# Performance work log

Measured on AMD Instinct MI355X. Metric: run time of the kernel, lower is better.

## Reference

```python
import jax, jax.numpy as jnp
import numpy as np

N_HEADS = 12


def setup_inputs() -> dict:
    key = jax.random.key(0)
    ks = jax.random.split(key, 4)
    B, S, D = 2, 2048, 768
    x = jax.random.normal(ks[0], (B, S, D), dtype=jnp.float32)
    # nn.Linear-style init scale ~ 1/sqrt(D) to keep logits reasonable
    scale = 1.0 / np.sqrt(D)
    Wq = jax.random.normal(ks[1], (D, D), dtype=jnp.float32) * scale
    Wk = jax.random.normal(ks[2], (D, D), dtype=jnp.float32) * scale
    Wv = jax.random.normal(ks[3], (D, D), dtype=jnp.float32) * scale
    bq = jnp.zeros((D,), jnp.float32)
    bk = jnp.zeros((D,), jnp.float32)
    bv = jnp.zeros((D,), jnp.float32)
    mask = jnp.ones((B, S), jnp.int32)
    return {"x": x, "Wq": Wq, "bq": bq, "Wk": Wk, "bk": bk,
            "Wv": Wv, "bv": bv, "mask": mask}


def reference(x, Wq, bq, Wk, bk, Wv, bv, mask):
    B, S, D = x.shape
    H = N_HEADS
    W = D // H
    # q,k,v: (B,S,D) -> (B,H,S,W)
    def proj(Wm, bm):
        return (x @ Wm.T + bm).reshape(B, S, H, W).transpose(0, 2, 1, 3)
    q, k, v = proj(Wq, bq), proj(Wk, bk), proj(Wv, bv)
    scores = jnp.einsum("bhsw,bhtw->bhst", q, k) / jnp.sqrt(
        jnp.asarray(W, x.dtype))
    # mask: (B,S) -> broadcast over query positions; 0 -> -1e20
    scores = jnp.where(mask[:, None, None, :] == 0,
                       jnp.asarray(-1e20, scores.dtype), scores)
    attn = jax.nn.softmax(scores, axis=-1)  # (B,H,S,S)
    # dropout p=0.0 (eval) -> identity
    ctx = jnp.einsum("bhst,bhtw->bhsw", attn, v)
    hidden = ctx.transpose(0, 2, 1, 3).reshape(B, S, D)
    return hidden
```

## Files before the change

### kernel.cpp

```cpp
#include <hip/hip_runtime.h>
#include <hip/hip_bf16.h>
#include <stdint.h>


typedef __attribute__((ext_vector_type(8))) short bf16x8;
typedef __attribute__((ext_vector_type(4))) float f32x4;
typedef __attribute__((ext_vector_type(16))) float f32x16;
typedef __attribute__((ext_vector_type(8))) unsigned short u16x8;

#define MFMA16(a, b, c) __builtin_amdgcn_mfma_f32_16x16x32_bf16((a), (b), (c), 0, 0, 0)
#define MFMA32(a, b, c) __builtin_amdgcn_mfma_f32_32x32x16_bf16((a), (b), (c), 0, 0, 0)
#define SWZ(row, colb) ((colb) ^ (((row) & 7) << 4))

union U32x4BF {
  unsigned u[4];
  bf16x8 v;
};

__device__ __forceinline__ void gl_lds16(const void* g, void* l) {
  __builtin_amdgcn_global_load_lds(
      (__attribute__((address_space(1))) void*)const_cast<void*>(g),
      (__attribute__((address_space(3))) void*)l, 16, 0, 0);
}

__device__ __forceinline__ unsigned short f2bf(float x) {
  unsigned int v = __float_as_uint(x);
  return (unsigned short)((v + 0x7fffu + ((v >> 16) & 1u)) >> 16);
}

__global__ __launch_bounds__(256) void cvt_all(
    const float* __restrict__ x, const float* __restrict__ wq,
    const float* __restrict__ wk, const float* __restrict__ wv,
    unsigned short* __restrict__ xb, unsigned short* __restrict__ wb) {
  int i = blockIdx.x * 256 + threadIdx.x;
  const float* s;
  unsigned short* d;
  int off;
  if (i < 393216)      { s = x;  d = xb;            off = i; }
  else if (i < 466944) { s = wq; d = wb;            off = i - 393216; }
  else if (i < 540672) { s = wk; d = wb + 589824;   off = i - 466944; }
  else                 { s = wv; d = wb + 1179648;  off = i - 540672; }
  const float4* sp = (const float4*)s + (size_t)off * 2;
  float4 a = sp[0], b2 = sp[1];
  u16x8 o;
  o[0] = f2bf(a.x); o[1] = f2bf(a.y); o[2] = f2bf(a.z); o[3] = f2bf(a.w);
  o[4] = f2bf(b2.x); o[5] = f2bf(b2.y); o[6] = f2bf(b2.z); o[7] = f2bf(b2.w);
  *((u16x8*)d + off) = o;
}

__global__ __launch_bounds__(256) void proj_gemm(
    const unsigned short* __restrict__ xb, const unsigned short* __restrict__ wb,
    const float* __restrict__ bq, const float* __restrict__ bk, const float* __restrict__ bv,
    unsigned short* __restrict__ qw, unsigned short* __restrict__ kw,
    unsigned short* __restrict__ vw) {
  __shared__ unsigned short lA[128 * 64];
  __shared__ unsigned short lB[128 * 64];
  const int t = threadIdx.x, lane = t & 63, wave = t >> 6;
  const int wr = wave >> 1, wc = wave & 1;
  const int mbase = blockIdx.x * 128;
  const int wsel = blockIdx.y / 6;
  const int nbase = (blockIdx.y % 6) * 128;
  const unsigned short* wmat = wb + (size_t)wsel * 589824;

  f32x4 acc[4][4];
#pragma unroll
  for (int i = 0; i < 4; i++)
#pragma unroll
    for (int j = 0; j < 4; j++) acc[i][j] = (f32x4){0.f, 0.f, 0.f, 0.f};

  char* lAc = (char*)lA;
  char* lBc = (char*)lB;

  for (int kt = 0; kt < 768; kt += 64) {
#pragma unroll
    for (int i = 0; i < 4; i++) {
      int p = t * 16 + i * 4096;
      int row = p >> 7, colb = p & 127;
      int scol = SWZ(row, colb);
      gl_lds16((const char*)xb + ((size_t)(mbase + row) * 768 + kt) * 2 + scol, lAc + p);
      gl_lds16((const char*)wmat + ((size_t)(nbase + row) * 768 + kt) * 2 + scol, lBc + p);
    }
    __syncthreads();

    bf16x8 af[2][4], bff[2][4];
#pragma unroll
    for (int mf = 0; mf < 4; mf++) {
      int row = wr * 64 + mf * 16 + (lane & 15);
#pragma unroll
      for (int kk = 0; kk < 2; kk++)
        af[kk][mf] = *(const bf16x8*)(lAc + row * 128 + SWZ(row, kk * 64 + (lane >> 4) * 16));
    }
#pragma unroll
    for (int nf = 0; nf < 4; nf++) {
      int row = wc * 64 + nf * 16 + (lane & 15);
#pragma unroll
      for (int kk = 0; kk < 2; kk++)
        bff[kk][nf] = *(const bf16x8*)(lBc + row * 128 + SWZ(row, kk * 64 + (lane >> 4) * 16));
    }
    if (wsel == 2) {
#pragma unroll
      for (int kk = 0; kk < 2; kk++)
#pragma unroll
        for (int mf = 0; mf < 4; mf++)
#pragma unroll
          for (int nf = 0; nf < 4; nf++)
            acc[mf][nf] = MFMA16(bff[kk][nf], af[kk][mf], acc[mf][nf]);
    } else {
#pragma unroll
      for (int kk = 0; kk < 2; kk++)
#pragma unroll
        for (int mf = 0; mf < 4; mf++)
#pragma unroll
          for (int nf = 0; nf < 4; nf++)
            acc[mf][nf] = MFMA16(af[kk][mf], bff[kk][nf], acc[mf][nf]);
    }
    __syncthreads();
  }

  const float QSCALE = 0.125f * 1.44269504089f;
  if (wsel == 2) {
#pragma unroll
    for (int nf = 0; nf < 4; nf++) {
#pragma unroll
      for (int mf = 0; mf < 4; mf++) {
#pragma unroll
        for (int r = 0; r < 4; r++) {
          int n = nbase + wc * 64 + nf * 16 + (lane >> 4) * 4 + r;
          int m = mbase + wr * 64 + mf * 16 + (lane & 15);
          int b_ = m >> 11, s = m & 2047;
          int h = n >> 6, wcol = n & 63;
          float val = acc[mf][nf][r] + bv[n];
          vw[(((size_t)b_ * 12 + h) * 64 + wcol) * 2048 + s] = f2bf(val);
        }
      }
    }
  } else {
    const float* bias = (wsel == 0) ? bq : bk;
#pragma unroll
    for (int nf = 0; nf < 4; nf++) {
      int n = nbase + wc * 64 + nf * 16 + (lane & 15);
      float bv_ = bias[n];
      int h = n >> 6, wcol = n & 63;
#pragma unroll
      for (int mf = 0; mf < 4; mf++) {
#pragma unroll
        for (int r = 0; r < 4; r++) {
          int m = mbase + wr * 64 + mf * 16 + (lane >> 4) * 4 + r;
          int b_ = m >> 11, s = m & 2047;
          float val = acc[mf][nf][r] + bv_;
          size_t bhh = (size_t)b_ * 12 + h;
          if (wsel == 0)
            qw[(bhh * 2048 + s) * 64 + wcol] = f2bf(val * QSCALE);
          else
            kw[(bhh * 2048 + s) * 64 + wcol] = f2bf(val);
        }
      }
    }
  }
}

__global__ __launch_bounds__(256, 4) void attn_kernel(
    const unsigned short* __restrict__ qw, const unsigned short* __restrict__ kw,
    const unsigned short* __restrict__ vw, const int* __restrict__ mask,
    float* __restrict__ out) {
  __shared__ __align__(16) char smem[33536];
  const int t = threadIdx.x, lane = t & 63, wave = t >> 6;
  const int wq = wave >> 1, wk = wave & 1;
  const int l31 = lane & 31, hl = lane >> 5;
  const int qb = blockIdx.x, bh = blockIdx.y;
  const int b = bh / 12, hh = bh - b * 12;

  {
    const int* mb = mask + (size_t)b * 2048 + t * 8;
    int4 a0 = *(const int4*)mb;
    int4 a1 = *(const int4*)(mb + 4);
    unsigned by = (unsigned)(a0.x != 0) | ((unsigned)(a0.y != 0) << 1) |
                  ((unsigned)(a0.z != 0) << 2) | ((unsigned)(a0.w != 0) << 3) |
                  ((unsigned)(a1.x != 0) << 4) | ((unsigned)(a1.y != 0) << 5) |
                  ((unsigned)(a1.z != 0) << 6) | ((unsigned)(a1.w != 0) << 7);
    smem[32768 + t] = (char)by;
  }

  bf16x8 qv[4];
  {
    int qrow = qb * 64 + wq * 32 + l31;
    const char* qp = (const char*)qw + ((size_t)bh * 2048 + qrow) * 128 + hl * 16;
#pragma unroll
    for (int s = 0; s < 4; s++) qv[s] = *(const bf16x8*)(qp + s * 32);
  }

  const char* kbaseg = (const char*)kw + (size_t)bh * 262144;
  const char* vbaseg = (const char*)vw + (size_t)bh * 262144;

  const int p0 = t * 16, p1 = t * 16 + 4096;
  const int r0 = p0 >> 7, s0 = SWZ(r0, p0 & 127);
  const int r1 = p1 >> 7, s1 = SWZ(r1, p1 & 127);

#define STAGE(IT, BUF)                                                                   \
  do {                                                                                   \
    int it_ = (IT);                                                                      \
    gl_lds16(kbaseg + (size_t)it_ * 8192 + r0 * 128 + s0, smem + (BUF) * 8192 + p0);     \
    gl_lds16(vbaseg + (size_t)r0 * 4096 + it_ * 128 + s0, smem + 16384 + (BUF) * 8192 + p0); \
    gl_lds16(kbaseg + (size_t)it_ * 8192 + r1 * 128 + s1, smem + (BUF) * 8192 + p1);     \
    gl_lds16(vbaseg + (size_t)r1 * 4096 + it_ * 128 + s1, smem + 16384 + (BUF) * 8192 + p1); \
  } while (0)

  f32x16 oacc[2];
#pragma unroll
  for (int wh = 0; wh < 2; wh++)
#pragma unroll
    for (int g = 0; g < 16; g++) oacc[wh][g] = 0.f;
  float lacc = 0.f;

  STAGE(0, 0);
  __syncthreads();

  for (int it = 0; it < 32; ++it) {
    if (it < 31) {
      STAGE(it + 1, (it + 1) & 1);
      asm volatile("s_waitcnt vmcnt(4)" ::: "memory");
    } else {
      asm volatile("s_waitcnt vmcnt(0)" ::: "memory");
    }
    __builtin_amdgcn_s_barrier();

    const char* lKc = smem + (it & 1) * 8192;
    const char* lVc = smem + 16384 + (it & 1) * 8192;

    f32x16 sc;
#pragma unroll
    for (int g = 0; g < 16; g++) sc[g] = 0.f;
    const int krow = wk * 32 + l31;
    __builtin_amdgcn_s_setprio(1);
#pragma unroll
    for (int s = 0; s < 4; s++) {
      bf16x8 kf = *(const bf16x8*)(lKc + krow * 128 + SWZ(krow, s * 32 + hl * 16));
      sc = MFMA32(kf, qv[s], sc);
    }
    __builtin_amdgcn_s_setprio(0);

    unsigned long long bal = *(const unsigned long long*)(smem + 32768 + it * 8);
    if (bal != ~0ull) {
#pragma unroll
      for (int g = 0; g < 16; g++) {
        int key = wk * 32 + 4 * hl + (g & 3) + 8 * (g >> 2);
        if (!((bal >> key) & 1)) sc[g] = -30000.f;
      }
    }

    float e[16];
#pragma unroll
    for (int g = 0; g < 16; g++)
      asm("v_exp_f32 %0, %1" : "=v"(e[g]) : "v"(sc[g]));
    lacc += (((e[0] + e[1]) + (e[2] + e[3])) + ((e[4] + e[5]) + (e[6] + e[7]))) +
            (((e[8] + e[9]) + (e[10] + e[11])) + ((e[12] + e[13]) + (e[14] + e[15])));
    unsigned pk[4][2];
#pragma unroll
    for (int m = 0; m < 4; m++) {
      asm("v_cvt_pk_bf16_f32 %0, %1, %2" : "=v"(pk[m][0]) : "v"(e[4 * m]), "v"(e[4 * m + 1]));
      asm("v_cvt_pk_bf16_f32 %0, %1, %2" : "=v"(pk[m][1]) : "v"(e[4 * m + 2]), "v"(e[4 * m + 3]));
    }
    U32x4BF apv[2];
#pragma unroll
    for (int sp = 0; sp < 2; sp++)
#pragma unroll
      for (int cp = 0; cp < 2; cp++) {
        unsigned xx = pk[2 * sp][cp], yy = pk[2 * sp + 1][cp];
        asm("v_permlane32_swap_b32 %0, %1" : "+v"(xx), "+v"(yy));
        apv[sp].u[cp] = xx;
        apv[sp].u[2 + cp] = yy;
      }

    __builtin_amdgcn_s_setprio(1);
#pragma unroll
    for (int wh = 0; wh < 2; wh++) {
      int vrow = wh * 32 + l31;
#pragma unroll
      for (int sp = 0; sp < 2; sp++) {
        bf16x8 vf = *(const bf16x8*)(lVc + vrow * 128 + SWZ(vrow, wk * 64 + sp * 32 + hl * 16));
        oacc[wh] = MFMA32(apv[sp].v, vf, oacc[wh]);
      }
    }
    __builtin_amdgcn_s_setprio(0);
    __builtin_amdgcn_s_barrier();
  }

  lacc += __shfl_xor(lacc, 32);
  if (lane < 32)
    *(float*)(smem + 33024 + (wk * 64 + wq * 32 + l31) * 4) = lacc;
  if (wk == 1) {
#pragma unroll
    for (int wh = 0; wh < 2; wh++) {
      int vrow = wh * 32 + l31;
#pragma unroll
      for (int m = 0; m < 4; m++) {
        f32x4 part = (f32x4){oacc[wh][4 * m], oacc[wh][4 * m + 1],
                             oacc[wh][4 * m + 2], oacc[wh][4 * m + 3]};
        *(f32x4*)(smem + wq * 8192 + vrow * 128 + SWZ(vrow, hl * 16 + m * 32)) = part;
      }
    }
  }
  __syncthreads();
  if (wk == 0) {
    float linv[16];
#pragma unroll
    for (int g = 0; g < 16; g++) {
      int qrow = 4 * hl + (g & 3) + 8 * (g >> 2);
      float l0 = *(const float*)(smem + 33024 + (wq * 32 + qrow) * 4);
      float l1 = *(const float*)(smem + 33024 + (64 + wq * 32 + qrow) * 4);
      linv[g] = __builtin_amdgcn_rcpf(l0 + l1);
    }
#pragma unroll
    for (int wh = 0; wh < 2; wh++) {
      int vrow = wh * 32 + l31;
#pragma unroll
      for (int m = 0; m < 4; m++) {
        f32x4 part = *(const f32x4*)(smem + wq * 8192 + vrow * 128 + SWZ(vrow, hl * 16 + m * 32));
#pragma unroll
        for (int r = 0; r < 4; r++) {
          int g = 4 * m + r;
          int qrow = 4 * hl + r + 8 * m;
          float val = (oacc[wh][g] + part[r]) * linv[g];
          out[((size_t)b * 2048 + qb * 64 + wq * 32 + qrow) * 768 + hh * 64 + wh * 32 + l31] =
              val;
        }
      }
    }
  }
#undef STAGE
}

extern "C" void kernel_launch(void* const* d_in, const int* in_sizes, int n_in,
                              void* d_out, int out_size, void* d_ws, size_t ws_size,
                              hipStream_t stream) {
  (void)in_sizes; (void)n_in; (void)out_size; (void)ws_size;
  const float* x  = (const float*)d_in[0];
  const float* Wq = (const float*)d_in[1];
  const float* bq = (const float*)d_in[2];
  const float* Wk = (const float*)d_in[3];
  const float* bk = (const float*)d_in[4];
  const float* Wv = (const float*)d_in[5];
  const float* bv = (const float*)d_in[6];
  const int* mask = (const int*)d_in[7];
  float* out = (float*)d_out;

  char* ws = (char*)d_ws;
  unsigned short* xb = (unsigned short*)(ws);
  unsigned short* wb = (unsigned short*)(ws + 6291456);
  unsigned short* qw = (unsigned short*)(ws + 9830400);
  unsigned short* kw = (unsigned short*)(ws + 16121856);
  unsigned short* vw = (unsigned short*)(ws + 22413312);

  cvt_all<<<2400, 256, 0, stream>>>(x, Wq, Wk, Wv, xb, wb);
  proj_gemm<<<dim3(32, 18), 256, 0, stream>>>(xb, wb, bq, bk, bv, qw, kw, vw);
  attn_kernel<<<dim3(32, 24), 256, 0, stream>>>(qw, kw, vw, mask, out);
}
```

Measured before the change: 88.39 us.

## Triple-buffer LDS pipelines in projection GEMM and attention with single barrier per step

The projection GEMM moves from a synchronous load-then-compute loop to a 3-stage software pipeline with async global-to-LDS prefetch, a K-step of 32, and a remapped LDS layout. The attention kernel also goes from double to triple buffering, which removes the trailing barrier per iteration, and its K/V tile layout is reorganized. The aim is to overlap memory loads with MFMA work and cut synchronization. In exchange, attention LDS rises to ~49KB and the occupancy hint of 4 blocks is dropped, which may lower occupancy.

```diff
diff --git a/kernel.cpp b/kernel.cpp
--- a/kernel.cpp
+++ b/kernel.cpp
@@ -53,14 +53,31 @@
     const float* __restrict__ bq, const float* __restrict__ bk, const float* __restrict__ bv,
     unsigned short* __restrict__ qw, unsigned short* __restrict__ kw,
     unsigned short* __restrict__ vw) {
-  __shared__ unsigned short lA[128 * 64];
-  __shared__ unsigned short lB[128 * 64];
+  __shared__ __align__(16) char psmem[49152];
   const int t = threadIdx.x, lane = t & 63, wave = t >> 6;
+  const int lo = lane & 15, hi = lane >> 4;
   const int wr = wave >> 1, wc = wave & 1;
   const int mbase = blockIdx.x * 128;
   const int wsel = blockIdx.y / 6;
   const int nbase = (blockIdx.y % 6) * 128;
-  const unsigned short* wmat = wb + (size_t)wsel * 589824;
+  const char* xc = (const char*)xb;
+  const char* wmc = (const char*)(wb + (size_t)wsel * 589824);
+
+  const int pp0 = t * 16, pp1 = t * 16 + 4096;
+  const int ar0 = pp0 >> 7, ac0 = (pp0 & 127) ^ ((ar0 & 7) << 4);
+  const int am0 = ((ac0 >> 6) << 6) + ar0, ak0 = ac0 & 63;
+  const int ar1 = pp1 >> 7, ac1 = (pp1 & 127) ^ ((ar1 & 7) << 4);
+  const int am1 = ((ac1 >> 6) << 6) + ar1, ak1 = ac1 & 63;
+
+#define PSTAGE(IT, BUF)                                                          \
+  do {                                                                           \
+    int it_ = (IT);                                                              \
+    char* lb = psmem + (BUF) * 16384;                                            \
+    gl_lds16(xc + (size_t)(mbase + am0) * 1536 + it_ * 64 + ak0, lb + pp0);      \
+    gl_lds16(xc + (size_t)(mbase + am1) * 1536 + it_ * 64 + ak1, lb + pp1);      \
+    gl_lds16(wmc + (size_t)(nbase + am0) * 1536 + it_ * 64 + ak0, lb + 8192 + pp0); \
+    gl_lds16(wmc + (size_t)(nbase + am1) * 1536 + it_ * 64 + ak1, lb + 8192 + pp1); \
+  } while (0)
 
   f32x4 acc[4][4];
 #pragma unroll
@@ -68,54 +85,45 @@
 #pragma unroll
     for (int j = 0; j < 4; j++) acc[i][j] = (f32x4){0.f, 0.f, 0.f, 0.f};
 
-  char* lAc = (char*)lA;
-  char* lBc = (char*)lB;
-
-  for (int kt = 0; kt < 768; kt += 64) {
-#pragma unroll
-    for (int i = 0; i < 4; i++) {
-      int p = t * 16 + i * 4096;
-      int row = p >> 7, colb = p & 127;
-      int scol = SWZ(row, colb);
-      gl_lds16((const char*)xb + ((size_t)(mbase + row) * 768 + kt) * 2 + scol, lAc + p);
-      gl_lds16((const char*)wmat + ((size_t)(nbase + row) * 768 + kt) * 2 + scol, lBc + p);
-    }
-    __syncthreads();
-
-    bf16x8 af[2][4], bff[2][4];
-#pragma unroll
-    for (int mf = 0; mf < 4; mf++) {
-      int row = wr * 64 + mf * 16 + (lane & 15);
-#pragma unroll
-      for (int kk = 0; kk < 2; kk++)
-        af[kk][mf] = *(const bf16x8*)(lAc + row * 128 + SWZ(row, kk * 64 + (lane >> 4) * 16));
-    }
-#pragma unroll
-    for (int nf = 0; nf < 4; nf++) {
-      int row = wc * 64 + nf * 16 + (lane & 15);
-#pragma unroll
-      for (int kk = 0; kk < 2; kk++)
-        bff[kk][nf] = *(const bf16x8*)(lBc + row * 128 + SWZ(row, kk * 64 + (lane >> 4) * 16));
-    }
+  const int axor = (lo & 7) << 4;
+  PSTAGE(0, 0);
+  int cur = 0, nxt = 1;
+  for (int it = 0; it < 24; ++it) {
+    if (it < 23) {
+      PSTAGE(it + 1, nxt);
+      asm volatile("s_waitcnt vmcnt(4)" ::: "memory");
+    } else {
+      asm volatile("s_waitcnt vmcnt(0)" ::: "memory");
+    }
+    __builtin_amdgcn_s_barrier();
+    const char* lA = psmem + cur * 16384;
+    const char* lB = lA + 8192;
+
+    bf16x8 af[4], bf[4];
+#pragma unroll
+    for (int mf = 0; mf < 4; mf++)
+      af[mf] = *(const bf16x8*)(lA + (mf * 16 + lo) * 128 + ((wr * 64 + hi * 16) ^ axor));
+#pragma unroll
+    for (int nf = 0; nf < 4; nf++)
+      bf[nf] = *(const bf16x8*)(lB + (nf * 16 + lo) * 128 + ((wc * 64 + hi * 16) ^ axor));
+
+    __builtin_amdgcn_s_setprio(1);
     if (wsel == 2) {
 #pragma unroll
-      for (int kk = 0; kk < 2; kk++)
-#pragma unroll
-        for (int mf = 0; mf < 4; mf++)
-#pragma unroll
-          for (int nf = 0; nf < 4; nf++)
-            acc[mf][nf] = MFMA16(bff[kk][nf], af[kk][mf], acc[mf][nf]);
+      for (int mf = 0; mf < 4; mf++)
+#pragma unroll
+        for (int nf = 0; nf < 4; nf++) acc[mf][nf] = MFMA16(bf[nf], af[mf], acc[mf][nf]);
     } else {
 #pragma unroll
-      for (int kk = 0; kk < 2; kk++)
-#pragma unroll
-        for (int mf = 0; mf < 4; mf++)
-#pragma unroll
-          for (int nf = 0; nf < 4; nf++)
-            acc[mf][nf] = MFMA16(af[kk][mf], bff[kk][nf], acc[mf][nf]);
-    }
-    __syncthreads();
-  }
+      for (int mf = 0; mf < 4; mf++)
+#pragma unroll
+        for (int nf = 0; nf < 4; nf++) acc[mf][nf] = MFMA16(af[mf], bf[nf], acc[mf][nf]);
+    }
+    __builtin_amdgcn_s_setprio(0);
+    cur = nxt;
+    nxt = (nxt == 2) ? 0 : nxt + 1;
+  }
+#undef PSTAGE
 
   const float QSCALE = 0.125f * 1.44269504089f;
   if (wsel == 2) {
@@ -125,8 +133,8 @@
       for (int mf = 0; mf < 4; mf++) {
 #pragma unroll
         for (int r = 0; r < 4; r++) {
-          int n = nbase + wc * 64 + nf * 16 + (lane >> 4) * 4 + r;
-          int m = mbase + wr * 64 + mf * 16 + (lane & 15);
+          int n = nbase + wc * 64 + nf * 16 + hi * 4 + r;
+          int m = mbase + wr * 64 + mf * 16 + lo;
           int b_ = m >> 11, s = m & 2047;
           int h = n >> 6, wcol = n & 63;
           float val = acc[mf][nf][r] + bv[n];
@@ -138,14 +146,14 @@
     const float* bias = (wsel == 0) ? bq : bk;
 #pragma unroll
     for (int nf = 0; nf < 4; nf++) {
-      int n = nbase + wc * 64 + nf * 16 + (lane & 15);
+      int n = nbase + wc * 64 + nf * 16 + lo;
       float bv_ = bias[n];
       int h = n >> 6, wcol = n & 63;
 #pragma unroll
       for (int mf = 0; mf < 4; mf++) {
 #pragma unroll
         for (int r = 0; r < 4; r++) {
-          int m = mbase + wr * 64 + mf * 16 + (lane >> 4) * 4 + r;
+          int m = mbase + wr * 64 + mf * 16 + hi * 4 + r;
           int b_ = m >> 11, s = m & 2047;
           float val = acc[mf][nf][r] + bv_;
           size_t bhh = (size_t)b_ * 12 + h;
@@ -159,11 +167,11 @@
   }
 }
 
-__global__ __launch_bounds__(256, 4) void attn_kernel(
+__global__ __launch_bounds__(256) void attn_kernel(
     const unsigned short* __restrict__ qw, const unsigned short* __restrict__ kw,
     const unsigned short* __restrict__ vw, const int* __restrict__ mask,
     float* __restrict__ out) {
-  __shared__ __align__(16) char smem[33536];
+  __shared__ __align__(16) char smem[49920];
   const int t = threadIdx.x, lane = t & 63, wave = t >> 6;
   const int wq = wave >> 1, wk = wave & 1;
   const int l31 = lane & 31, hl = lane >> 5;
@@ -178,8 +186,9 @@
                   ((unsigned)(a0.z != 0) << 2) | ((unsigned)(a0.w != 0) << 3) |
                   ((unsigned)(a1.x != 0) << 4) | ((unsigned)(a1.y != 0) << 5) |
                   ((unsigned)(a1.z != 0) << 6) | ((unsigned)(a1.w != 0) << 7);
-    smem[32768 + t] = (char)by;
-  }
+    smem[49152 + t] = (char)by;
+  }
+  asm volatile("s_waitcnt lgkmcnt(0)" ::: "memory");
 
   bf16x8 qv[4];
   {
@@ -193,16 +202,19 @@
   const char* vbaseg = (const char*)vw + (size_t)bh * 262144;
 
   const int p0 = t * 16, p1 = t * 16 + 4096;
-  const int r0 = p0 >> 7, s0 = SWZ(r0, p0 & 127);
-  const int r1 = p1 >> 7, s1 = SWZ(r1, p1 & 127);
-
-#define STAGE(IT, BUF)                                                                   \
-  do {                                                                                   \
-    int it_ = (IT);                                                                      \
-    gl_lds16(kbaseg + (size_t)it_ * 8192 + r0 * 128 + s0, smem + (BUF) * 8192 + p0);     \
-    gl_lds16(vbaseg + (size_t)r0 * 4096 + it_ * 128 + s0, smem + 16384 + (BUF) * 8192 + p0); \
-    gl_lds16(kbaseg + (size_t)it_ * 8192 + r1 * 128 + s1, smem + (BUF) * 8192 + p1);     \
-    gl_lds16(vbaseg + (size_t)r1 * 4096 + it_ * 128 + s1, smem + 16384 + (BUF) * 8192 + p1); \
+  const int r0 = p0 >> 9, c0 = (p0 >> 7) & 3, o0 = (p0 & 127) ^ ((r0 & 7) << 4);
+  const int ks0 = (c0 * 16 + r0) * 128 + o0, vs0 = (c0 * 16 + r0) * 4096 + o0;
+  const int r1 = p1 >> 9, c1 = (p1 >> 7) & 3, o1 = (p1 & 127) ^ ((r1 & 7) << 4);
+  const int ks1 = (c1 * 16 + r1) * 128 + o1, vs1 = (c1 * 16 + r1) * 4096 + o1;
+
+#define STAGE(IT, BUF)                                                     \
+  do {                                                                     \
+    int it_ = (IT);                                                        \
+    char* kb = smem + (BUF) * 16384;                                       \
+    gl_lds16(kbaseg + (size_t)it_ * 8192 + ks0, kb + p0);                  \
+    gl_lds16(kbaseg + (size_t)it_ * 8192 + ks1, kb + p1);                  \
+    gl_lds16(vbaseg + (size_t)it_ * 128 + vs0, kb + 8192 + p0);            \
+    gl_lds16(vbaseg + (size_t)it_ * 128 + vs1, kb + 8192 + p1);            \
   } while (0)
 
   f32x16 oacc[2];
@@ -212,34 +224,36 @@
     for (int g = 0; g < 16; g++) oacc[wh][g] = 0.f;
   float lacc = 0.f;
 
+  const int kbl = (l31 & 15) * 512 + (wk * 2 + (l31 >> 4)) * 128;
+  const int rxor = (l31 & 7) << 4;
+  const int hl16 = hl * 16;
+
   STAGE(0, 0);
-  __syncthreads();
-
+  int cur = 0, nxt = 1;
   for (int it = 0; it < 32; ++it) {
     if (it < 31) {
-      STAGE(it + 1, (it + 1) & 1);
+      STAGE(it + 1, nxt);
       asm volatile("s_waitcnt vmcnt(4)" ::: "memory");
     } else {
       asm volatile("s_waitcnt vmcnt(0)" ::: "memory");
     }
     __builtin_amdgcn_s_barrier();
 
-    const char* lKc = smem + (it & 1) * 8192;
-    const char* lVc = smem + 16384 + (it & 1) * 8192;
+    const char* lKc = smem + cur * 16384;
+    const char* lVc = lKc + 8192;
 
     f32x16 sc;
 #pragma unroll
     for (int g = 0; g < 16; g++) sc[g] = 0.f;
-    const int krow = wk * 32 + l31;
     __builtin_amdgcn_s_setprio(1);
 #pragma unroll
     for (int s = 0; s < 4; s++) {
-      bf16x8 kf = *(const bf16x8*)(lKc + krow * 128 + SWZ(krow, s * 32 + hl * 16));
+      bf16x8 kf = *(const bf16x8*)(lKc + kbl + ((s * 32 + hl16) ^ rxor));
       sc = MFMA32(kf, qv[s], sc);
     }
     __builtin_amdgcn_s_setprio(0);
 
-    unsigned long long bal = *(const unsigned long long*)(smem + 32768 + it * 8);
+    unsigned long long bal = *(const unsigned long long*)(smem + 49152 + it * 8);
     if (bal != ~0ull) {
 #pragma unroll
       for (int g = 0; g < 16; g++) {
@@ -274,20 +288,21 @@
     __builtin_amdgcn_s_setprio(1);
 #pragma unroll
     for (int wh = 0; wh < 2; wh++) {
-      int vrow = wh * 32 + l31;
+      int vbl = (l31 & 15) * 512 + (wh * 2 + (l31 >> 4)) * 128;
 #pragma unroll
       for (int sp = 0; sp < 2; sp++) {
-        bf16x8 vf = *(const bf16x8*)(lVc + vrow * 128 + SWZ(vrow, wk * 64 + sp * 32 + hl * 16));
+        bf16x8 vf = *(const bf16x8*)(lVc + vbl + ((wk * 64 + sp * 32 + hl16) ^ rxor));
         oacc[wh] = MFMA32(apv[sp].v, vf, oacc[wh]);
       }
     }
     __builtin_amdgcn_s_setprio(0);
-    __builtin_amdgcn_s_barrier();
+    cur = nxt;
+    nxt = (nxt == 2) ? 0 : nxt + 1;
   }
 
   lacc += __shfl_xor(lacc, 32);
   if (lane < 32)
-    *(float*)(smem + 33024 + (wk * 64 + wq * 32 + l31) * 4) = lacc;
+    *(float*)(smem + 49408 + (wk * 64 + wq * 32 + l31) * 4) = lacc;
   if (wk == 1) {
 #pragma unroll
     for (int wh = 0; wh < 2; wh++) {
@@ -306,8 +321,8 @@
 #pragma unroll
     for (int g = 0; g < 16; g++) {
       int qrow = 4 * hl + (g & 3) + 8 * (g >> 2);
-      float l0 = *(const float*)(smem + 33024 + (wq * 32 + qrow) * 4);
-      float l1 = *(const float*)(smem + 33024 + (64 + wq * 32 + qrow) * 4);
+      float l0 = *(const float*)(smem + 49408 + (wq * 32 + qrow) * 4);
+      float l1 = *(const float*)(smem + 49408 + (64 + wq * 32 + qrow) * 4);
       linv[g] = __builtin_amdgcn_rcpf(l0 + l1);
     }
 #pragma unroll
```

After: 86.74 us. No clear change (-1.9%).
